# Optimization experiments

Hardware: AMD Instinct MI355X
Metric: run time of the kernel (lower is better)

## Reference

```python
import jax, jax.numpy as jnp
import numpy as np

EPS = 1e-5

def conv1d(x, w, b, stride, pad):
    # x: [N, Cin, L], w: [Cout, Cin, K]
    out = jax.lax.conv_general_dilated(x, w, (stride,), [(pad, pad)], dimension_numbers=('NCH', 'OIH', 'NCH'))
    return out + b[None, :, None]

def bn_eval(x, g, b):
    # BatchNorm1d in eval mode with running_mean=0, running_var=1
    return x * (g / jnp.sqrt(1.0 + EPS))[None, :, None] + b[None, :, None]

def maxpool3(x):
    return jax.lax.reduce_window(x, -jnp.inf, jax.lax.max, (1, 1, 3), (1, 1, 3), 'VALID')

def layer_norm(x, g, b):
    m = x.mean(-1, keepdims=True)
    v = ((x - m) ** 2).mean(-1, keepdims=True)
    return (x - m) / jnp.sqrt(v + EPS) * g + b

def lstm_dir(x, w_ih, w_hh, b_ih, b_hh, reverse):
    # x: [B, S, I]; torch gate order i, f, g, o
    B = x.shape[0]; H = w_hh.shape[1]
    xs = jnp.einsum('bsi,gi->bsg', x, w_ih) + b_ih + b_hh
    if reverse:
        xs = xs[:, ::-1]
    def step(carry, xt):
        h, c = carry
        gates = xt + h @ w_hh.T
        i, f, g, o = jnp.split(gates, 4, axis=-1)
        c = jax.nn.sigmoid(f) * c + jax.nn.sigmoid(i) * jnp.tanh(g)
        h = jax.nn.sigmoid(o) * jnp.tanh(c)
        return (h, c), h
    init = (jnp.zeros((B, H), x.dtype), jnp.zeros((B, H), x.dtype))
    _, hs = jax.lax.scan(step, init, jnp.swapaxes(xs, 0, 1))
    hs = jnp.swapaxes(hs, 0, 1)
    return hs[:, ::-1] if reverse else hs

def setup_inputs() -> dict:
    key = jax.random.key(0)
    ks = iter(jax.random.split(key, 48))
    def rn(shape, s=0.05):
        return jax.random.normal(next(ks), shape, jnp.float32) * s
    B, S, C, T, F0, Hg, Hl, NC = 64, 20, 8, 3000, 64, 128, 256, 5
    return dict(
        x=jax.random.normal(next(ks), (B, S, C, T), jnp.float32),
        edge_index=jax.random.randint(next(ks), (2, 56), 0, C, jnp.int32),
        conv1_w=rn((16, 1, 7)), conv1_b=jnp.zeros(16), bn1_g=jnp.ones(16), bn1_b=jnp.zeros(16),
        conv2_w=rn((32, 16, 5)), conv2_b=jnp.zeros(32), bn2_g=jnp.ones(32), bn2_b=jnp.zeros(32),
        conv3_w=rn((F0, 32, 3)), conv3_b=jnp.zeros(F0), bn3_g=jnp.ones(F0), bn3_b=jnp.zeros(F0),
        gcn0_w=rn((Hg, F0)), gcn0_b=jnp.zeros(Hg),
        gcn1_w=rn((Hg, Hg)), gcn1_b=jnp.zeros(Hg),
        gnn_ln_g=jnp.ones(Hg), gnn_ln_b=jnp.zeros(Hg),
        w_ih_l0=rn((4 * Hl, Hg)), w_hh_l0=rn((4 * Hl, Hl)), b_ih_l0=jnp.zeros(4 * Hl), b_hh_l0=jnp.zeros(4 * Hl),
        w_ih_l0r=rn((4 * Hl, Hg)), w_hh_l0r=rn((4 * Hl, Hl)), b_ih_l0r=jnp.zeros(4 * Hl), b_hh_l0r=jnp.zeros(4 * Hl),
        w_ih_l1=rn((4 * Hl, 2 * Hl)), w_hh_l1=rn((4 * Hl, Hl)), b_ih_l1=jnp.zeros(4 * Hl), b_hh_l1=jnp.zeros(4 * Hl),
        w_ih_l1r=rn((4 * Hl, 2 * Hl)), w_hh_l1r=rn((4 * Hl, Hl)), b_ih_l1r=jnp.zeros(4 * Hl), b_hh_l1r=jnp.zeros(4 * Hl),
        lstm_ln_g=jnp.ones(2 * Hl), lstm_ln_b=jnp.zeros(2 * Hl),
        cls_w=rn((NC, 2 * Hl)), cls_b=jnp.zeros(NC),
    )

def reference(x, edge_index, conv1_w, conv1_b, bn1_g, bn1_b, conv2_w, conv2_b, bn2_g, bn2_b, conv3_w, conv3_b, bn3_g, bn3_b, gcn0_w, gcn0_b, gcn1_w, gcn1_b, gnn_ln_g, gnn_ln_b, w_ih_l0, w_hh_l0, b_ih_l0, b_hh_l0, w_ih_l0r, w_hh_l0r, b_ih_l0r, b_hh_l0r, w_ih_l1, w_hh_l1, b_ih_l1, b_hh_l1, w_ih_l1r, w_hh_l1r, b_ih_l1r, b_hh_l1r, lstm_ln_g, lstm_ln_b, cls_w, cls_b):
    B, S, C, T = x.shape
    # batched per-channel CNN over all B*S epochs at once (original: python double loop)
    h = x.reshape(B * S * C, 1, T)
    h = maxpool3(jax.nn.relu(bn_eval(conv1d(h, conv1_w, conv1_b, 2, 3), bn1_g, bn1_b)))
    h = maxpool3(jax.nn.relu(bn_eval(conv1d(h, conv2_w, conv2_b, 2, 2), bn2_g, bn2_b)))
    h = jax.nn.relu(bn_eval(conv1d(h, conv3_w, conv3_b, 1, 1), bn3_g, bn3_b))
    feats = h.mean(-1).reshape(B * S, C, -1)  # AdaptiveAvgPool1d(1) -> [BS, C, 64]
    # GCNConv normalized adjacency: D^-1/2 (A + I) D^-1/2, graph is tiny (C nodes) so dense is exact and efficient
    src, dst = edge_index[0], edge_index[1]
    A = jnp.zeros((C, C), x.dtype).at[dst, src].add(1.0) + jnp.eye(C, dtype=x.dtype)
    dinv = 1.0 / jnp.sqrt(A.sum(1))
    An = A * dinv[:, None] * dinv[None, :]
    g1 = jax.nn.relu(jnp.einsum('ij,bjf->bif', An, feats @ gcn0_w.T) + gcn0_b)  # dropout off (eval)
    g2 = jnp.einsum('ij,bjf->bif', An, g1 @ gcn1_w.T) + gcn1_b
    g2 = layer_norm(g2, gnn_ln_g, gnn_ln_b)
    emb = g2.mean(1).reshape(B, S, -1)  # mean over nodes -> [B, S, 128]
    l0 = jnp.concatenate([lstm_dir(emb, w_ih_l0, w_hh_l0, b_ih_l0, b_hh_l0, False),
                          lstm_dir(emb, w_ih_l0r, w_hh_l0r, b_ih_l0r, b_hh_l0r, True)], -1)
    l1 = jnp.concatenate([lstm_dir(l0, w_ih_l1, w_hh_l1, b_ih_l1, b_hh_l1, False),
                          lstm_dir(l0, w_ih_l1r, w_hh_l1r, b_ih_l1r, b_hh_l1r, True)], -1)
    out = layer_norm(l1, lstm_ln_g, lstm_ln_b)
    return out @ cls_w.T + cls_b  # [B, S, 5]
```

## Files before the change

kernel.cpp:

```cpp
#include <hip/hip_runtime.h>
#include <hip/hip_bf16.h>

#define DEVI __device__ __forceinline__

typedef _Float16 h2f16 __attribute__((ext_vector_type(2)));
typedef _Float16 f16x4 __attribute__((ext_vector_type(4)));
typedef _Float16 f16x8 __attribute__((ext_vector_type(8)));
typedef float    f32x4 __attribute__((ext_vector_type(4)));
union U4H { uint4 u; h2f16 h[4]; };
union F8  { f16x8 v8; f16x4 v4[2]; };

DEVI float sigf(float x){ return 1.f/(1.f + __expf(-x)); }
DEVI float tanh_f(float x){
  float ax = fabsf(x);
  float e = __expf(-2.f*ax);
  float t = (1.f - e)/(1.f + e);
  return copysignf(t, x);
}
DEVI h2f16 hmax2(h2f16 a, h2f16 b){
  h2f16 r; r[0] = a[0] > b[0] ? a[0] : b[0]; r[1] = a[1] > b[1] ? a[1] : b[1]; return r;
}

__global__ __launch_bounds__(256) void k_prep(
  const int* __restrict__ ei, float* __restrict__ An,
  const float* __restrict__ w2, const float* __restrict__ w3,
  const float* __restrict__ bg2, const float* __restrict__ bg3,
  _Float16* __restrict__ bw2f, _Float16* __restrict__ bw3f,
  const float* __restrict__ a0, const float* __restrict__ a1,
  const float* __restrict__ a2, const float* __restrict__ a3,
  const float* __restrict__ a4, const float* __restrict__ a5,
  _Float16* __restrict__ o0, _Float16* __restrict__ o1,
  _Float16* __restrict__ o2, _Float16* __restrict__ o3,
  _Float16* __restrict__ o4, _Float16* __restrict__ o5,
  const float* __restrict__ whh0, const float* __restrict__ whh0r,
  const float* __restrict__ whh1, const float* __restrict__ whh1r,
  h2f16* __restrict__ wt0f, h2f16* __restrict__ wt0r,
  h2f16* __restrict__ wt1f, h2f16* __restrict__ wt1r)
{
  const int bid = blockIdx.x, tid = threadIdx.x;
  if (bid == 0){
    __shared__ float A[64];
    __shared__ float dinv[8];
    if (tid<64) A[tid] = ((tid>>3)==(tid&7)) ? 1.f : 0.f;
    __syncthreads();
    if (tid==0){
      for (int e=0;e<56;e++){ int s=ei[e], d=ei[56+e]; A[d*8+s] += 1.f; }
    }
    __syncthreads();
    if (tid<8){ float s=0.f; for (int j=0;j<8;j++) s+=A[tid*8+j]; dinv[tid]=rsqrtf(s); }
    __syncthreads();
    if (tid<64) An[tid] = A[tid]*dinv[tid>>3]*dinv[tid&7];
    return;
  }
  if (bid <= 24){
    const int i = (bid-1)*256 + tid;
    const float rs = rsqrtf(1.f+1e-5f);
    if (i < 3072){
      const int j = i&7, m = (i>>3)&15, g = (i>>7)&3, nt = (i>>9)&1, s = i>>10;
      const int kk = 32*s + 8*g + j;
      const int k = kk >> 4, ic = kk & 15, oc = nt*16 + m;
      bw2f[i] = (_Float16)((k < 5 ? w2[oc*80 + ic*5 + k] : 0.f) * (bg2[oc]*rs));
    }
    if (i < 6144){
      const int j = i&7, m = (i>>3)&15, g = (i>>7)&3, wv = (i>>9)&3, s = i>>11;
      const int kk = 32*s + 8*g + j;
      const int k = kk >> 5, ic = kk & 31, oc = wv*16 + m;
      bw3f[i] = (_Float16)(w3[oc*96 + ic*3 + k] * (bg3[oc]*rs));
    }
    return;
  }
  if (bid <= 5240){
    const int i = (bid-25)*256 + tid;
    if      (i <  131072) o0[i] = (_Float16)a0[i];
    else if (i <  262144) o1[i-131072] = (_Float16)a1[i-131072];
    else if (i <  786432) o2[i-262144] = (_Float16)a2[i-262144];
    else if (i < 1310720) o3[i-786432] = (_Float16)a3[i-786432];
    else if (i < 1318912) o4[i-1310720] = (_Float16)a4[i-1310720];
    else if (i < 1335296) o5[i-1318912] = (_Float16)a5[i-1318912];
    return;
  }
  {
    const int idx = (bid-5241)*256 + tid;
    const int which = idx >> 17, i = idx & 131071;
    const int g = i & 1023, jp = i >> 10;
    const float* in = (which==0) ? whh0 : (which==1) ? whh0r : (which==2) ? whh1 : whh1r;
    h2f16* outp    = (which==0) ? wt0f : (which==1) ? wt0r  : (which==2) ? wt1f : wt1r;
    h2f16 p;
    p[0] = (_Float16)in[g*256 + 2*jp];
    p[1] = (_Float16)in[g*256 + 2*jp + 1];
    outp[(long)jp*1024 + g] = p;
  }
}

__global__ __launch_bounds__(512,8) void k_conv(
    const float* __restrict__ x,
    const float* __restrict__ w1g, const float* __restrict__ c1b,
    const float* __restrict__ bg1, const float* __restrict__ bb1,
    const _Float16* __restrict__ bw2f,
    const float* __restrict__ c2b, const float* __restrict__ bg2, const float* __restrict__ bb2,
    const _Float16* __restrict__ bw3f,
    const float* __restrict__ c3b, const float* __restrict__ bg3, const float* __restrict__ bb3,
    _Float16* __restrict__ feats)
{
  __shared__ __align__(16) unsigned char smb[38592];
  __shared__ h2f16 w1p[16][4];
  __shared__ float kb1o[16], kb2o[32], kb3o[64];
  __shared__ float redc[8][16];
  h2f16* sxh = reinterpret_cast<h2f16*>(smb + 20160);
  const int tid = threadIdx.x;
  const long sig = blockIdx.x;
  const float* xg = x + sig*3000;

  {
    const float4* xg4 = reinterpret_cast<const float4*>(xg);
    for (int i=tid; i<750; i+=512){
      float4 v = xg4[i];
      h2f16 p0; p0[0]=(_Float16)v.x; p0[1]=(_Float16)v.y;
      h2f16 p1; p1[0]=(_Float16)v.z; p1[1]=(_Float16)v.w;
      sxh[2*i+2] = p0; sxh[2*i+3] = p1;
    }
    if (tid<3){
      h2f16 z; z[0]=(_Float16)0.f; z[1]=(_Float16)0.f;
      sxh[tid<2 ? tid : 1502] = z;
    }
    if (tid<32){
      const int rr = tid>>3, cp = tid&7;
      const int row = (rr<2) ? rr : (500+rr);
      h2f16 z; z[0]=(_Float16)0.f; z[1]=(_Float16)0.f;
      *reinterpret_cast<h2f16*>(smb + row*40 + 4*cp) = z;
    }
    const float rs = rsqrtf(1.f+1e-5f);
    if (tid<64){
      const int c = tid>>2, j = tid&3;
      const float s = bg1[c]*rs;
      h2f16 p;
      if (j==0){ p[0]=(_Float16)0.f; p[1]=(_Float16)(w1g[c*7+0]*s); }
      else     { p[0]=(_Float16)(w1g[c*7+2*j-1]*s); p[1]=(_Float16)(w1g[c*7+2*j]*s); }
      w1p[c][j] = p;
    }
    if (tid<16) kb1o[tid] = c1b[tid]*(bg1[tid]*rs) + bb1[tid];
    if (tid<32) kb2o[tid] = c2b[tid]*(bg2[tid]*rs) + bb2[tid];
    if (tid<64) kb3o[tid] = c3b[tid]*(bg3[tid]*rs) + bb3[tid];
  }
  __syncthreads();

  {
    const int cp = tid & 7;
    h2f16 wpa[4], wpb[4];
    #pragma unroll
    for (int j=0;j<4;j++){ wpa[j] = w1p[2*cp][j]; wpb[j] = w1p[2*cp+1][j]; }
    const float oa = kb1o[2*cp], ob = kb1o[2*cp+1];
    for (int u = tid>>3; u<500; u+=64){
      h2f16 xq[6];
      #pragma unroll
      for (int r=0;r<6;r++) xq[r] = sxh[3*u + r];
      float a0=0.f,a1=0.f,a2=0.f,b0=0.f,b1=0.f,b2=0.f;
      #pragma unroll
      for (int j=0;j<4;j++){
        a0 = __builtin_amdgcn_fdot2(xq[j],   wpa[j], a0, false);
        a1 = __builtin_amdgcn_fdot2(xq[j+1], wpa[j], a1, false);
        a2 = __builtin_amdgcn_fdot2(xq[j+2], wpa[j], a2, false);
        b0 = __builtin_amdgcn_fdot2(xq[j],   wpb[j], b0, false);
        b1 = __builtin_amdgcn_fdot2(xq[j+1], wpb[j], b1, false);
        b2 = __builtin_amdgcn_fdot2(xq[j+2], wpb[j], b2, false);
      }
      const float ya = fmaxf(fmaxf(fmaxf(a0,a1),a2) + oa, 0.f);
      const float yb = fmaxf(fmaxf(fmaxf(b0,b1),b2) + ob, 0.f);
      h2f16 p; p[0]=(_Float16)ya; p[1]=(_Float16)yb;
      *reinterpret_cast<h2f16*>(smb + (u+2)*40 + 4*cp) = p;
    }
  }
  __syncthreads();

  const int wv = tid >> 6, lane = tid & 63;
  const int m = lane & 15, g = lane >> 4;

  {
    const int nt = wv & 1;
    f16x8 bf[3];
    #pragma unroll
    for (int s=0;s<3;s++)
      bf[s] = *reinterpret_cast<const f16x8*>(&bw2f[(((s*2+nt)*4+g)*16+m)*8]);
    const int oc = nt*16 + m;
    const float of = kb2o[oc];
    #pragma unroll
    for (int i=0;i<4;i++){
      const int mt = (wv>>1) + 4*i;
      const int trow = mt*16 + m;
      f32x4 acc = {0.f,0.f,0.f,0.f};
      #pragma unroll
      for (int s=0;s<3;s++){
        const int kk = 32*s + 8*g;
        const int k = kk >> 4;
        const int ab = 80*trow + 40*k + 16*(g&1);
        F8 a;
        a.v4[0] = *reinterpret_cast<const f16x4*>(smb + ab);
        a.v4[1] = *reinterpret_cast<const f16x4*>(smb + ab + 8);
        acc = __builtin_amdgcn_mfma_f32_16x16x32_f16(a.v8, bf[s], acc, 0,0,0);
      }
      #pragma unroll
      for (int r=0;r<4;r++){
        const int t = mt*16 + 4*g + r;
        const float z = fmaxf(acc[r] + of, 0.f);
        *reinterpret_cast<_Float16*>(smb + 20160 + t*72 + 2*oc) = (_Float16)z;
      }
    }
  }
  __syncthreads();

  {
    if (tid < 240){
      const int rr = tid >> 4, cc = tid & 15;
      const int row = (rr == 0) ? 0 : (83 + rr);
      h2f16 z; z[0]=(_Float16)0.f; z[1]=(_Float16)0.f;
      *reinterpret_cast<h2f16*>(smb + row*80 + 4*cc) = z;
    }
    for (int i=tid; i<1328; i+=512){
      const int u = i >> 4, cc = i & 15;
      h2f16 a = *reinterpret_cast<const h2f16*>(smb + 20160 + (3*u)*72 + 4*cc);
      h2f16 b = *reinterpret_cast<const h2f16*>(smb + 20160 + (3*u+1)*72 + 4*cc);
      h2f16 c = *reinterpret_cast<const h2f16*>(smb + 20160 + (3*u+2)*72 + 4*cc);
      *reinterpret_cast<h2f16*>(smb + (u+1)*80 + 4*cc) = hmax2(hmax2(a,b), c);
    }
  }
  __syncthreads();

  {
    const int nt = wv & 3;
    f16x8 bf[3];
    #pragma unroll
    for (int s=0;s<3;s++)
      bf[s] = *reinterpret_cast<const f16x8*>(&bw3f[(((s*4+nt)*4+g)*16+m)*8]);
    const int oc = nt*16 + m;
    const float of = kb3o[oc];
    float macc = 0.f;
    #pragma unroll
    for (int q=0;q<3;q++){
      const int mt = (wv>>2) + 2*q;
      const int trow = mt*16 + m;
      f32x4 acc = {0.f,0.f,0.f,0.f};
      #pragma unroll
      for (int s=0;s<3;s++){
        f16x8 af = *reinterpret_cast<const f16x8*>(smb + (trow + s)*80 + 16*g);
        acc = __builtin_amdgcn_mfma_f32_16x16x32_f16(af, bf[s], acc, 0,0,0);
      }
      #pragma unroll
      for (int r=0;r<4;r++){
        const int t = mt*16 + 4*g + r;
        if (t < 83) macc += fmaxf(acc[r] + of, 0.f);
      }
    }
    macc += __shfl_xor(macc, 16);
    macc += __shfl_xor(macc, 32);
    if (lane < 16) redc[wv][m] = macc;
  }
  __syncthreads();
  if (tid < 64)
    feats[sig*64 + tid] = (_Float16)((redc[tid>>4][tid&15] + redc[(tid>>4)+4][tid&15]) * (1.f/83.f));
}

__global__ __launch_bounds__(256) void k_gcn1(
  const _Float16* __restrict__ X, const _Float16* __restrict__ W,
  const float* __restrict__ An, const float* __restrict__ b0,
  _Float16* __restrict__ g1, int K)
{
  __shared__ __align__(16) unsigned char lds[17408];
  __shared__ float ans[64];
  unsigned char* Xs = lds;
  unsigned char* Ws = lds + 4608;
  float* Cs = reinterpret_cast<float*>(lds);
  const int tid = threadIdx.x;
  const int m0 = blockIdx.y*64, n0 = blockIdx.x*64;
  const int wv = tid>>6, lane = tid&63, m = lane&15, g = lane>>4;
  const int sr = tid>>2, sq = tid&3;
  if (tid<64) ans[tid] = An[tid];
  f32x4 acc[4] = {{0.f,0.f,0.f,0.f},{0.f,0.f,0.f,0.f},{0.f,0.f,0.f,0.f},{0.f,0.f,0.f,0.f}};
  for (int k0=0; k0<K; k0+=32){
    uint4 xa = *reinterpret_cast<const uint4*>(X + (long)(m0+sr)*K + k0 + sq*8);
    uint4 wa = *reinterpret_cast<const uint4*>(W + (long)(n0+sr)*K + k0 + sq*8);
    __syncthreads();
    *reinterpret_cast<uint4*>(Xs + sr*72 + sq*16) = xa;
    *reinterpret_cast<uint4*>(Ws + sr*72 + sq*16) = wa;
    __syncthreads();
    f16x8 af = *reinterpret_cast<const f16x8*>(Xs + (wv*16+m)*72 + g*16);
    #pragma unroll
    for (int nt=0;nt<4;nt++){
      f16x8 bf = *reinterpret_cast<const f16x8*>(Ws + (nt*16+m)*72 + g*16);
      acc[nt] = __builtin_amdgcn_mfma_f32_16x16x32_f16(af, bf, acc[nt], 0,0,0);
    }
  }
  __syncthreads();
  #pragma unroll
  for (int nt=0;nt<4;nt++)
    #pragma unroll
    for (int r=0;r<4;r++)
      Cs[(wv*16 + g*4 + r)*68 + nt*16 + m] = acc[nt][r];
  __syncthreads();
  for (int idx=tid; idx<512; idx+=256){
    const int gg = idx>>6, j = idx&63;
    float t[8];
    #pragma unroll
    for (int c=0;c<8;c++) t[c] = Cs[(gg*8+c)*68 + j];
    const float bj = b0[n0+j];
    #pragma unroll
    for (int i=0;i<8;i++){
      float s = bj;
      #pragma unroll
      for (int c=0;c<8;c++) s += ans[i*8+c]*t[c];
      g1[(long)(m0 + gg*8 + i)*128 + n0 + j] = (_Float16)fmaxf(s, 0.f);
    }
  }
}

__global__ __launch_bounds__(256) void k_gcn2(
  const _Float16* __restrict__ X, const _Float16* __restrict__ W,
  const float* __restrict__ An, const float* __restrict__ b1,
  const float* __restrict__ lng, const float* __restrict__ lnb,
  _Float16* __restrict__ emb)
{
  __shared__ __align__(16) unsigned char lds[33792];
  __shared__ float ans[64];
  unsigned char* Xs = lds;
  unsigned char* Ws = lds + 4608;
  float* Cs = reinterpret_cast<float*>(lds);
  const int tid = threadIdx.x;
  const int m0 = blockIdx.x*64;
  const int wv = tid>>6, lane = tid&63, m = lane&15, g = lane>>4;
  const int sr = tid>>2, sq = tid&3;
  if (tid<64) ans[tid] = An[tid];
  f32x4 acc[8] = {};
  for (int k0=0; k0<128; k0+=32){
    uint4 xa = *reinterpret_cast<const uint4*>(X + (long)(m0+sr)*128 + k0 + sq*8);
    uint4 wa0 = *reinterpret_cast<const uint4*>(W + (long)(tid>>1)*128 + k0 + (tid&1)*16);
    uint4 wa1 = *reinterpret_cast<const uint4*>(W + (long)(tid>>1)*128 + k0 + (tid&1)*16 + 8);
    __syncthreads();
    *reinterpret_cast<uint4*>(Xs + sr*72 + sq*16) = xa;
    *reinterpret_cast<uint4*>(Ws + (tid>>1)*72 + (tid&1)*32) = wa0;
    *reinterpret_cast<uint4*>(Ws + (tid>>1)*72 + (tid&1)*32 + 16) = wa1;
    __syncthreads();
    f16x8 af = *reinterpret_cast<const f16x8*>(Xs + (wv*16+m)*72 + g*16);
    #pragma unroll
    for (int nt=0;nt<8;nt++){
      f16x8 bf = *reinterpret_cast<const f16x8*>(Ws + (nt*16+m)*72 + g*16);
      acc[nt] = __builtin_amdgcn_mfma_f32_16x16x32_f16(af, bf, acc[nt], 0,0,0);
    }
  }
  __syncthreads();
  #pragma unroll
  for (int nt=0;nt<8;nt++)
    #pragma unroll
    for (int r=0;r<4;r++)
      Cs[(wv*16 + g*4 + r)*132 + nt*16 + m] = acc[nt][r];
  __syncthreads();
  {
    const int s = tid>>5, l = tid&31;
    float g2v[8][4];
    #pragma unroll
    for (int jj=0;jj<4;jj++){
      const int j = l + jj*32;
      float t[8];
      #pragma unroll
      for (int c=0;c<8;c++) t[c] = Cs[(s*8+c)*132 + j];
      const float bj = b1[j];
      #pragma unroll
      for (int i=0;i<8;i++){
        float v = bj;
        #pragma unroll
        for (int c=0;c<8;c++) v += ans[i*8+c]*t[c];
        g2v[i][jj] = v;
      }
    }
    float mi[8], ri[8];
    #pragma unroll
    for (int i=0;i<8;i++){
      float sm=0.f, sq2=0.f;
      #pragma unroll
      for (int jj=0;jj<4;jj++){ sm += g2v[i][jj]; sq2 += g2v[i][jj]*g2v[i][jj]; }
      #pragma unroll
      for (int off=16; off>=1; off>>=1){ sm += __shfl_xor(sm, off); sq2 += __shfl_xor(sq2, off); }
      const float mu = sm*(1.f/128.f);
      mi[i] = mu;
      ri[i] = rsqrtf(sq2*(1.f/128.f) - mu*mu + 1e-5f);
    }
    #pragma unroll
    for (int jj=0;jj<4;jj++){
      const int j = l + jj*32;
      float a = 0.f;
      #pragma unroll
      for (int i=0;i<8;i++) a += (g2v[i][jj]-mi[i])*ri[i];
      emb[(long)(blockIdx.x*8 + s)*128 + j] = (_Float16)(lng[j]*a*0.125f + lnb[j]);
    }
  }
}

__global__ __launch_bounds__(256) void k_gemm_mf2(
  const _Float16* __restrict__ X,
  const _Float16* __restrict__ Wa, const _Float16* __restrict__ Wb,
  const float* __restrict__ b1a, const float* __restrict__ b2a,
  const float* __restrict__ b1b, const float* __restrict__ b2b,
  float* __restrict__ C, int co, int M, int N, int K, int ldc)
{
  __shared__ __align__(16) unsigned char lds[128*72];
  unsigned char* Xs = lds;
  unsigned char* Ws = lds + 64*72;
  const int z = blockIdx.z;
  const _Float16* W = z ? Wb : Wa;
  const float* b1 = z ? b1b : b1a;
  const float* b2 = z ? b2b : b2a;
  float* Cz = C + (z ? co : 0);
  const int tid = threadIdx.x;
  const int m0 = blockIdx.y*64, n0 = blockIdx.x*64;
  const int wv = tid>>6, lane = tid&63, m = lane&15, g = lane>>4;
  const int sr = tid>>2, sq = tid&3;
  f32x4 acc[4] = {{0.f,0.f,0.f,0.f},{0.f,0.f,0.f,0.f},{0.f,0.f,0.f,0.f},{0.f,0.f,0.f,0.f}};
  for (int k0=0; k0<K; k0+=32){
    uint4 xa = *reinterpret_cast<const uint4*>(X + (long)(m0+sr)*K + k0 + sq*8);
    uint4 wa = *reinterpret_cast<const uint4*>(W + (long)(n0+sr)*K + k0 + sq*8);
    __syncthreads();
    *reinterpret_cast<uint4*>(Xs + sr*72 + sq*16) = xa;
    *reinterpret_cast<uint4*>(Ws + sr*72 + sq*16) = wa;
    __syncthreads();
    f16x8 af = *reinterpret_cast<const f16x8*>(Xs + (wv*16+m)*72 + g*16);
    #pragma unroll
    for (int nt=0;nt<4;nt++){
      f16x8 bf = *reinterpret_cast<const f16x8*>(Ws + (nt*16+m)*72 + g*16);
      acc[nt] = __builtin_amdgcn_mfma_f32_16x16x32_f16(af, bf, acc[nt], 0,0,0);
    }
  }
  #pragma unroll
  for (int nt=0;nt<4;nt++){
    const int col = n0 + nt*16 + m;
    float bias = b1[col] + b2[col];
    #pragma unroll
    for (int r=0;r<4;r++)
      Cz[(long)(m0 + wv*16 + g*4 + r)*ldc + col] = acc[nt][r] + bias;
  }
}

__global__ __launch_bounds__(1024) void k_lstm(
    const float* __restrict__ xs,
    const h2f16* __restrict__ wtf,
    const h2f16* __restrict__ wtr,
    float* __restrict__ outf,
    _Float16* __restrict__ outh)
{
  const int S = 20;
  const int b = blockIdx.x >> 1, dir = blockIdx.x & 1;
  const h2f16* wt = dir ? wtr : wtf;
  __shared__ float part[4][1024];
  __shared__ _Float16 hsh[256];
  __shared__ __align__(16) unsigned char wlds[131072];
  const int tid = threadIdx.x;
  const int jg = tid >> 8, r = tid & 255, grow = r*4;
  uint4 wreg[16];
  #pragma unroll
  for (int jp=0;jp<16;jp++)
    wreg[jp] = *reinterpret_cast<const uint4*>(
        reinterpret_cast<const unsigned int*>(wt + (long)(jg*32+jp)*1024 + grow));
  {
    const uint4* wsrc = reinterpret_cast<const uint4*>(wt);
    uint4* wdst = reinterpret_cast<uint4*>(wlds);
    for (int i=tid; i<8192; i+=1024){
      const int src = (i < 4096) ? (4096 + i) : (12288 + (i - 4096));
      wdst[i] = wsrc[src];
    }
  }
  if (tid < 256) hsh[tid] = (_Float16)0.f;
  float cc = 0.f;
  __syncthreads();
  const h2f16* hp2 = reinterpret_cast<const h2f16*>(hsh);
  for (int st=0; st<S; ++st){
    const int t = dir ? (S-1-st) : st;
    float a0=0.f,a1=0.f,a2=0.f,a3=0.f;
    #pragma unroll
    for (int jp=0; jp<16; ++jp){
      const h2f16 hv = hp2[jg*32 + jp];
      U4H w; w.u = wreg[jp];
      a0 = __builtin_amdgcn_fdot2(hv, w.h[0], a0, false);
      a1 = __builtin_amdgcn_fdot2(hv, w.h[1], a1, false);
      a2 = __builtin_amdgcn_fdot2(hv, w.h[2], a2, false);
      a3 = __builtin_amdgcn_fdot2(hv, w.h[3], a3, false);
    }
    if (jg < 2){
      #pragma unroll 8
      for (int jp=16; jp<32; ++jp){
        const h2f16 hv = hp2[jg*32 + jp];
        U4H w; w.u = *reinterpret_cast<const uint4*>(
            wlds + (long)(jg*16 + (jp-16))*4096 + grow*4);
        a0 = __builtin_amdgcn_fdot2(hv, w.h[0], a0, false);
        a1 = __builtin_amdgcn_fdot2(hv, w.h[1], a1, false);
        a2 = __builtin_amdgcn_fdot2(hv, w.h[2], a2, false);
        a3 = __builtin_amdgcn_fdot2(hv, w.h[3], a3, false);
      }
    } else {
      #pragma unroll 8
      for (int jp=16; jp<32; ++jp){
        const h2f16 hv = hp2[jg*32 + jp];
        U4H w; w.u = *reinterpret_cast<const uint4*>(
            reinterpret_cast<const unsigned int*>(wt + (long)(jg*32+jp)*1024 + grow));
        a0 = __builtin_amdgcn_fdot2(hv, w.h[0], a0, false);
        a1 = __builtin_amdgcn_fdot2(hv, w.h[1], a1, false);
        a2 = __builtin_amdgcn_fdot2(hv, w.h[2], a2, false);
        a3 = __builtin_amdgcn_fdot2(hv, w.h[3], a3, false);
      }
    }
    *reinterpret_cast<float4*>(&part[jg][grow]) = make_float4(a0,a1,a2,a3);
    __syncthreads();
    if (tid < 256){
      const float* xrow = xs + ((long)b*S + t)*2048 + dir*1024;
      float g0 = xrow[tid]
               + (part[0][tid]      + part[1][tid])      + (part[2][tid]      + part[3][tid]);
      float g1 = xrow[256+tid]
               + (part[0][256+tid]  + part[1][256+tid])  + (part[2][256+tid]  + part[3][256+tid]);
      float g2 = xrow[512+tid]
               + (part[0][512+tid]  + part[1][512+tid])  + (part[2][512+tid]  + part[3][512+tid]);
      float g3 = xrow[768+tid]
               + (part[0][768+tid]  + part[1][768+tid])  + (part[2][768+tid]  + part[3][768+tid]);
      cc = sigf(g1)*cc + sigf(g0)*tanh_f(g2);
      const float h = sigf(g3)*tanh_f(cc);
      hsh[tid] = (_Float16)h;
      const long o = ((long)b*S + t)*512 + dir*256 + tid;
      if (outf) outf[o] = h;
      if (outh) outh[o] = (_Float16)h;
    }
    __syncthreads();
  }
}

__global__ __launch_bounds__(128) void k_lncls(
  const float* __restrict__ in, const float* __restrict__ g,
  const float* __restrict__ b, const float* __restrict__ cw,
  const float* __restrict__ cb, float* __restrict__ out)
{
  const int row = blockIdx.x, tid = threadIdx.x;
  __shared__ float sred[4];
  __shared__ float cred[2][5];
  float4 v = *reinterpret_cast<const float4*>(in + (long)row*512 + tid*4);
  float s  = v.x+v.y+v.z+v.w;
  float sq = v.x*v.x+v.y*v.y+v.z*v.z+v.w*v.w;
  #pragma unroll
  for (int off=32; off>=1; off>>=1){ s += __shfl_xor(s, off); sq += __shfl_xor(sq, off); }
  const int wv = tid>>6;
  if ((tid&63)==0){ sred[wv*2]=s; sred[wv*2+1]=sq; }
  __syncthreads();
  const float S = sred[0]+sred[2], SQ = sred[1]+sred[3];
  const float m = S*(1.f/512.f);
  const float rstd = rsqrtf(SQ*(1.f/512.f) - m*m + 1e-5f);
  float4 gg = *reinterpret_cast<const float4*>(g + tid*4);
  float4 bb = *reinterpret_cast<const float4*>(b + tid*4);
  const float n0 = (v.x-m)*rstd*gg.x + bb.x;
  const float n1 = (v.y-m)*rstd*gg.y + bb.y;
  const float n2 = (v.z-m)*rstd*gg.z + bb.z;
  const float n3 = (v.w-m)*rstd*gg.w + bb.w;
  #pragma unroll
  for (int nc=0; nc<5; ++nc){
    float4 w = *reinterpret_cast<const float4*>(cw + nc*512 + tid*4);
    float p = n0*w.x + n1*w.y + n2*w.z + n3*w.w;
    #pragma unroll
    for (int off=32; off>=1; off>>=1) p += __shfl_xor(p, off);
    if ((tid&63)==0) cred[wv][nc] = p;
  }
  __syncthreads();
  if (tid < 5) out[(long)row*5 + tid] = cred[0][tid] + cred[1][tid] + cb[tid];
}

extern "C" void kernel_launch(void* const* d_in, const int* in_sizes, int n_in,
                              void* d_out, int out_size, void* d_ws, size_t ws_size,
                              hipStream_t stream)
{
  const float* x     = (const float*)d_in[0];
  const int*   ei    = (const int*)d_in[1];
  const float* w1    = (const float*)d_in[2];
  const float* c1b   = (const float*)d_in[3];
  const float* bg1   = (const float*)d_in[4];
  const float* bb1   = (const float*)d_in[5];
  const float* w2    = (const float*)d_in[6];
  const float* c2b   = (const float*)d_in[7];
  const float* bg2   = (const float*)d_in[8];
  const float* bb2   = (const float*)d_in[9];
  const float* w3    = (const float*)d_in[10];
  const float* c3b   = (const float*)d_in[11];
  const float* bg3   = (const float*)d_in[12];
  const float* bb3   = (const float*)d_in[13];
  const float* gcn0w = (const float*)d_in[14];
  const float* gcn0b = (const float*)d_in[15];
  const float* gcn1w = (const float*)d_in[16];
  const float* gcn1b = (const float*)d_in[17];
  const float* lng   = (const float*)d_in[18];
  const float* lnb   = (const float*)d_in[19];
  const float* wih0  = (const float*)d_in[20];
  const float* whh0  = (const float*)d_in[21];
  const float* bih0  = (const float*)d_in[22];
  const float* bhh0  = (const float*)d_in[23];
  const float* wih0r = (const float*)d_in[24];
  const float* whh0r = (const float*)d_in[25];
  const float* bih0r = (const float*)d_in[26];
  const float* bhh0r = (const float*)d_in[27];
  const float* wih1  = (const float*)d_in[28];
  const float* whh1  = (const float*)d_in[29];
  const float* bih1  = (const float*)d_in[30];
  const float* bhh1  = (const float*)d_in[31];
  const float* wih1r = (const float*)d_in[32];
  const float* whh1r = (const float*)d_in[33];
  const float* bih1r = (const float*)d_in[34];
  const float* bhh1r = (const float*)d_in[35];
  const float* lstmg = (const float*)d_in[36];
  const float* lstmb = (const float*)d_in[37];
  const float* clsw  = (const float*)d_in[38];
  const float* clsb  = (const float*)d_in[39];
  float* ws  = (float*)d_ws;
  float* out = (float*)d_out;

  float*    An      = ws + 0;
  _Float16* bw2f    = (_Float16*)(ws + 64);
  _Float16* bw3f    = (_Float16*)(ws + 1600);
  _Float16* feats16 = (_Float16*)(ws + 4672);
  _Float16* g1b16   = (_Float16*)(ws + 332352);
  _Float16* emb16   = (_Float16*)(ws + 987712);
  _Float16* l0h     = (_Float16*)(ws + 1069632);
  _Float16* w0f     = (_Float16*)(ws + 1397312);
  _Float16* w0rf    = (_Float16*)(ws + 1462848);
  _Float16* w1f     = (_Float16*)(ws + 1528384);
  _Float16* w1rf    = (_Float16*)(ws + 1790528);
  _Float16* gw0f    = (_Float16*)(ws + 2052672);
  _Float16* gw1f    = (_Float16*)(ws + 2056768);
  h2f16*    wt0f    = (h2f16*)(ws + 2064960);
  h2f16*    wt0r    = (h2f16*)(ws + 2196032);
  h2f16*    wt1f    = (h2f16*)(ws + 2327104);
  h2f16*    wt1r    = (h2f16*)(ws + 2458176);
  float*    l1f     = ws + 2589248;
  float*    xs      = ws + 3244608;

  k_prep<<<7289, 256, 0, stream>>>(ei, An, w2, w3, bg2, bg3, bw2f, bw3f,
                                   wih0, wih0r, wih1, wih1r, gcn0w, gcn1w,
                                   w0f, w0rf, w1f, w1rf, gw0f, gw1f,
                                   whh0, whh0r, whh1, whh1r,
                                   wt0f, wt0r, wt1f, wt1r);
  k_conv<<<10240, 512, 0, stream>>>(x, w1,c1b,bg1,bb1, bw2f,c2b,bg2,bb2,
                                    bw3f,c3b,bg3,bb3, feats16);

  k_gcn1<<<dim3(2, 160), 256, 0, stream>>>(feats16, gw0f, An, gcn0b, g1b16, 64);
  k_gcn2<<<160, 256, 0, stream>>>(g1b16, gw1f, An, gcn1b, lng, lnb, emb16);

  k_gemm_mf2<<<dim3(16, 20, 2), 256, 0, stream>>>(emb16, w0f, w0rf,
      bih0, bhh0, bih0r, bhh0r, xs, 1024, 1280, 1024, 128, 2048);
  k_lstm<<<128, 1024, 0, stream>>>(xs, wt0f, wt0r, nullptr, l0h);

  k_gemm_mf2<<<dim3(16, 20, 2), 256, 0, stream>>>(l0h, w1f, w1rf,
      bih1, bhh1, bih1r, bhh1r, xs, 1024, 1280, 1024, 512, 2048);
  k_lstm<<<128, 1024, 0, stream>>>(xs, wt1f, wt1r, l1f, nullptr);

  k_lncls<<<1280, 128, 0, stream>>>(l1f, lstmg, lstmb, clsw, clsb, out);
}
```

Before: 293.1 us.

## Fuse GCN layers, store LSTM gate inputs in fp16, tile weight transpose

The two GCN kernels become one, which keeps the intermediate layer in LDS instead of writing it to global memory. The input-projection GEMM now uses 128-row tiles with 512 threads and writes fp16 gate pre-activations, and the LSTM kernels read them as fp16. This halves that traffic but reduces precision. The recurrent-weight transpose in the prep kernel now goes through an LDS tile so global reads are coalesced, and the launch uses fewer blocks.

```diff
diff --git a/kernel.cpp b/kernel.cpp
--- a/kernel.cpp
+++ b/kernel.cpp
@@ -80,15 +80,28 @@
     return;
   }
   {
-    const int idx = (bid-5241)*256 + tid;
-    const int which = idx >> 17, i = idx & 131071;
-    const int g = i & 1023, jp = i >> 10;
+    __shared__ float tl[64][65];
+    const int t = bid - 5241;
+    const int which = t >> 6, tile = t & 63;
+    const int tg = tile >> 2, tc = tile & 3;
     const float* in = (which==0) ? whh0 : (which==1) ? whh0r : (which==2) ? whh1 : whh1r;
     h2f16* outp    = (which==0) ? wt0f : (which==1) ? wt0r  : (which==2) ? wt1f : wt1r;
-    h2f16 p;
-    p[0] = (_Float16)in[g*256 + 2*jp];
-    p[1] = (_Float16)in[g*256 + 2*jp + 1];
-    outp[(long)jp*1024 + g] = p;
+    #pragma unroll
+    for (int p=0;p<16;p++){
+      const int lin = p*256 + tid;
+      const int r = lin >> 6, cc = lin & 63;
+      tl[r][cc] = in[(tg*64 + r)*256 + tc*64 + cc];
+    }
+    __syncthreads();
+    #pragma unroll
+    for (int p=0;p<8;p++){
+      const int lin = p*256 + tid;
+      const int gl = lin & 63, jph = lin >> 6;
+      h2f16 v;
+      v[0] = (_Float16)tl[gl][2*jph];
+      v[1] = (_Float16)tl[gl][2*jph+1];
+      outp[(long)(tc*32 + jph)*1024 + tg*64 + gl] = v;
+    }
   }
 }
 
@@ -259,98 +272,90 @@
     feats[sig*64 + tid] = (_Float16)((redc[tid>>4][tid&15] + redc[(tid>>4)+4][tid&15]) * (1.f/83.f));
 }
 
-__global__ __launch_bounds__(256) void k_gcn1(
-  const _Float16* __restrict__ X, const _Float16* __restrict__ W,
+__global__ __launch_bounds__(256) void k_gcn(
+  const _Float16* __restrict__ feats, const _Float16* __restrict__ W0,
+  const _Float16* __restrict__ W1,
   const float* __restrict__ An, const float* __restrict__ b0,
-  _Float16* __restrict__ g1, int K)
+  const float* __restrict__ b1, const float* __restrict__ lng,
+  const float* __restrict__ lnb, _Float16* __restrict__ emb)
 {
-  __shared__ __align__(16) unsigned char lds[17408];
+  __shared__ __align__(16) unsigned char lds[66304];
   __shared__ float ans[64];
-  unsigned char* Xs = lds;
-  unsigned char* Ws = lds + 4608;
-  float* Cs = reinterpret_cast<float*>(lds);
-  const int tid = threadIdx.x;
-  const int m0 = blockIdx.y*64, n0 = blockIdx.x*64;
-  const int wv = tid>>6, lane = tid&63, m = lane&15, g = lane>>4;
-  const int sr = tid>>2, sq = tid&3;
-  if (tid<64) ans[tid] = An[tid];
-  f32x4 acc[4] = {{0.f,0.f,0.f,0.f},{0.f,0.f,0.f,0.f},{0.f,0.f,0.f,0.f},{0.f,0.f,0.f,0.f}};
-  for (int k0=0; k0<K; k0+=32){
-    uint4 xa = *reinterpret_cast<const uint4*>(X + (long)(m0+sr)*K + k0 + sq*8);
-    uint4 wa = *reinterpret_cast<const uint4*>(W + (long)(n0+sr)*K + k0 + sq*8);
-    __syncthreads();
-    *reinterpret_cast<uint4*>(Xs + sr*72 + sq*16) = xa;
-    *reinterpret_cast<uint4*>(Ws + sr*72 + sq*16) = wa;
-    __syncthreads();
-    f16x8 af = *reinterpret_cast<const f16x8*>(Xs + (wv*16+m)*72 + g*16);
-    #pragma unroll
-    for (int nt=0;nt<4;nt++){
-      f16x8 bf = *reinterpret_cast<const f16x8*>(Ws + (nt*16+m)*72 + g*16);
-      acc[nt] = __builtin_amdgcn_mfma_f32_16x16x32_f16(af, bf, acc[nt], 0,0,0);
-    }
-  }
-  __syncthreads();
-  #pragma unroll
-  for (int nt=0;nt<4;nt++)
-    #pragma unroll
-    for (int r=0;r<4;r++)
-      Cs[(wv*16 + g*4 + r)*68 + nt*16 + m] = acc[nt][r];
-  __syncthreads();
-  for (int idx=tid; idx<512; idx+=256){
-    const int gg = idx>>6, j = idx&63;
-    float t[8];
-    #pragma unroll
-    for (int c=0;c<8;c++) t[c] = Cs[(gg*8+c)*68 + j];
-    const float bj = b0[n0+j];
-    #pragma unroll
-    for (int i=0;i<8;i++){
-      float s = bj;
-      #pragma unroll
-      for (int c=0;c<8;c++) s += ans[i*8+c]*t[c];
-      g1[(long)(m0 + gg*8 + i)*128 + n0 + j] = (_Float16)fmaxf(s, 0.f);
-    }
-  }
-}
-
-__global__ __launch_bounds__(256) void k_gcn2(
-  const _Float16* __restrict__ X, const _Float16* __restrict__ W,
-  const float* __restrict__ An, const float* __restrict__ b1,
-  const float* __restrict__ lng, const float* __restrict__ lnb,
-  _Float16* __restrict__ emb)
-{
-  __shared__ __align__(16) unsigned char lds[33792];
-  __shared__ float ans[64];
-  unsigned char* Xs = lds;
-  unsigned char* Ws = lds + 4608;
-  float* Cs = reinterpret_cast<float*>(lds);
+  unsigned char* Xs  = lds;
+  unsigned char* Ws0 = lds + 4608;
+  float*         Cs  = reinterpret_cast<float*>(lds + 13824);
+  unsigned char* W1s = lds + 13824;
+  unsigned char* g1h = lds + 48896;
   const int tid = threadIdx.x;
   const int m0 = blockIdx.x*64;
   const int wv = tid>>6, lane = tid&63, m = lane&15, g = lane>>4;
   const int sr = tid>>2, sq = tid&3;
   if (tid<64) ans[tid] = An[tid];
-  f32x4 acc[8] = {};
-  for (int k0=0; k0<128; k0+=32){
-    uint4 xa = *reinterpret_cast<const uint4*>(X + (long)(m0+sr)*128 + k0 + sq*8);
-    uint4 wa0 = *reinterpret_cast<const uint4*>(W + (long)(tid>>1)*128 + k0 + (tid&1)*16);
-    uint4 wa1 = *reinterpret_cast<const uint4*>(W + (long)(tid>>1)*128 + k0 + (tid&1)*16 + 8);
-    __syncthreads();
-    *reinterpret_cast<uint4*>(Xs + sr*72 + sq*16) = xa;
-    *reinterpret_cast<uint4*>(Ws + (tid>>1)*72 + (tid&1)*32) = wa0;
-    *reinterpret_cast<uint4*>(Ws + (tid>>1)*72 + (tid&1)*32 + 16) = wa1;
-    __syncthreads();
-    f16x8 af = *reinterpret_cast<const f16x8*>(Xs + (wv*16+m)*72 + g*16);
-    #pragma unroll
-    for (int nt=0;nt<8;nt++){
-      f16x8 bf = *reinterpret_cast<const f16x8*>(Ws + (nt*16+m)*72 + g*16);
-      acc[nt] = __builtin_amdgcn_mfma_f32_16x16x32_f16(af, bf, acc[nt], 0,0,0);
-    }
-  }
-  __syncthreads();
-  #pragma unroll
-  for (int nt=0;nt<8;nt++)
-    #pragma unroll
-    for (int r=0;r<4;r++)
-      Cs[(wv*16 + g*4 + r)*132 + nt*16 + m] = acc[nt][r];
+  {
+    f32x4 acc[8] = {};
+    for (int k0=0; k0<64; k0+=32){
+      uint4 xa  = *reinterpret_cast<const uint4*>(feats + (long)(m0+sr)*64 + k0 + sq*8);
+      uint4 wa0 = *reinterpret_cast<const uint4*>(W0 + (long)sr*64 + k0 + sq*8);
+      uint4 wa1 = *reinterpret_cast<const uint4*>(W0 + (long)(sr+64)*64 + k0 + sq*8);
+      __syncthreads();
+      *reinterpret_cast<uint4*>(Xs + sr*72 + sq*16) = xa;
+      *reinterpret_cast<uint4*>(Ws0 + sr*72 + sq*16) = wa0;
+      *reinterpret_cast<uint4*>(Ws0 + (sr+64)*72 + sq*16) = wa1;
+      __syncthreads();
+      f16x8 af = *reinterpret_cast<const f16x8*>(Xs + (wv*16+m)*72 + g*16);
+      #pragma unroll
+      for (int nt=0;nt<8;nt++){
+        f16x8 bf = *reinterpret_cast<const f16x8*>(Ws0 + (nt*16+m)*72 + g*16);
+        acc[nt] = __builtin_amdgcn_mfma_f32_16x16x32_f16(af, bf, acc[nt], 0,0,0);
+      }
+    }
+    __syncthreads();
+    #pragma unroll
+    for (int nt=0;nt<8;nt++)
+      #pragma unroll
+      for (int r=0;r<4;r++)
+        Cs[(wv*16 + g*4 + r)*132 + nt*16 + m] = acc[nt][r];
+  }
+  __syncthreads();
+  for (int idx=tid; idx<1024; idx+=256){
+    const int gg = idx>>7, j = idx&127;
+    float t[8];
+    #pragma unroll
+    for (int c=0;c<8;c++) t[c] = Cs[(gg*8+c)*132 + j];
+    const float bj = b0[j];
+    #pragma unroll
+    for (int i=0;i<8;i++){
+      float s = bj;
+      #pragma unroll
+      for (int c=0;c<8;c++) s += ans[i*8+c]*t[c];
+      *reinterpret_cast<_Float16*>(g1h + (gg*8+i)*272 + j*2) = (_Float16)fmaxf(s, 0.f);
+    }
+  }
+  __syncthreads();
+  for (int i2=tid; i2<2048; i2+=256){
+    const int row = i2>>4, q = i2&15;
+    *reinterpret_cast<uint4*>(W1s + row*272 + q*16) =
+        *reinterpret_cast<const uint4*>(W1 + (long)row*128 + q*8);
+  }
+  __syncthreads();
+  {
+    f32x4 acc2[8] = {};
+    #pragma unroll
+    for (int kc=0;kc<4;kc++){
+      f16x8 af = *reinterpret_cast<const f16x8*>(g1h + (wv*16+m)*272 + kc*64 + g*16);
+      #pragma unroll
+      for (int nt=0;nt<8;nt++){
+        f16x8 bf = *reinterpret_cast<const f16x8*>(W1s + (nt*16+m)*272 + kc*64 + g*16);
+        acc2[nt] = __builtin_amdgcn_mfma_f32_16x16x32_f16(af, bf, acc2[nt], 0,0,0);
+      }
+    }
+    __syncthreads();
+    #pragma unroll
+    for (int nt=0;nt<8;nt++)
+      #pragma unroll
+      for (int r=0;r<4;r++)
+        Cs[(wv*16 + g*4 + r)*132 + nt*16 + m] = acc2[nt][r];
+  }
   __syncthreads();
   {
     const int s = tid>>5, l = tid&31;
@@ -393,32 +398,34 @@
   }
 }
 
-__global__ __launch_bounds__(256) void k_gemm_mf2(
+__global__ __launch_bounds__(512) void k_gemm_mf2(
   const _Float16* __restrict__ X,
   const _Float16* __restrict__ Wa, const _Float16* __restrict__ Wb,
   const float* __restrict__ b1a, const float* __restrict__ b2a,
   const float* __restrict__ b1b, const float* __restrict__ b2b,
-  float* __restrict__ C, int co, int M, int N, int K, int ldc)
+  _Float16* __restrict__ C, int K)
 {
-  __shared__ __align__(16) unsigned char lds[128*72];
+  __shared__ __align__(16) unsigned char lds[13824];
   unsigned char* Xs = lds;
-  unsigned char* Ws = lds + 64*72;
+  unsigned char* Ws = lds + 9216;
   const int z = blockIdx.z;
   const _Float16* W = z ? Wb : Wa;
   const float* b1 = z ? b1b : b1a;
   const float* b2 = z ? b2b : b2a;
-  float* Cz = C + (z ? co : 0);
+  _Float16* Cz = C + (z ? 1024 : 0);
   const int tid = threadIdx.x;
-  const int m0 = blockIdx.y*64, n0 = blockIdx.x*64;
+  const int m0 = blockIdx.y*128, n0 = blockIdx.x*64;
   const int wv = tid>>6, lane = tid&63, m = lane&15, g = lane>>4;
   const int sr = tid>>2, sq = tid&3;
   f32x4 acc[4] = {{0.f,0.f,0.f,0.f},{0.f,0.f,0.f,0.f},{0.f,0.f,0.f,0.f},{0.f,0.f,0.f,0.f}};
   for (int k0=0; k0<K; k0+=32){
     uint4 xa = *reinterpret_cast<const uint4*>(X + (long)(m0+sr)*K + k0 + sq*8);
-    uint4 wa = *reinterpret_cast<const uint4*>(W + (long)(n0+sr)*K + k0 + sq*8);
+    uint4 wa = make_uint4(0,0,0,0);
+    if (tid < 256)
+      wa = *reinterpret_cast<const uint4*>(W + (long)(n0+sr)*K + k0 + sq*8);
     __syncthreads();
     *reinterpret_cast<uint4*>(Xs + sr*72 + sq*16) = xa;
-    *reinterpret_cast<uint4*>(Ws + sr*72 + sq*16) = wa;
+    if (tid < 256) *reinterpret_cast<uint4*>(Ws + sr*72 + sq*16) = wa;
     __syncthreads();
     f16x8 af = *reinterpret_cast<const f16x8*>(Xs + (wv*16+m)*72 + g*16);
     #pragma unroll
@@ -433,12 +440,12 @@
     float bias = b1[col] + b2[col];
     #pragma unroll
     for (int r=0;r<4;r++)
-      Cz[(long)(m0 + wv*16 + g*4 + r)*ldc + col] = acc[nt][r] + bias;
+      Cz[(long)(m0 + wv*16 + g*4 + r)*2048 + col] = (_Float16)(acc[nt][r] + bias);
   }
 }
 
 __global__ __launch_bounds__(1024) void k_lstm(
-    const float* __restrict__ xs,
+    const _Float16* __restrict__ xs,
     const h2f16* __restrict__ wtf,
     const h2f16* __restrict__ wtr,
     float* __restrict__ outf,
@@ -507,14 +514,14 @@
     *reinterpret_cast<float4*>(&part[jg][grow]) = make_float4(a0,a1,a2,a3);
     __syncthreads();
     if (tid < 256){
-      const float* xrow = xs + ((long)b*S + t)*2048 + dir*1024;
-      float g0 = xrow[tid]
+      const _Float16* xrow = xs + ((long)b*S + t)*2048 + dir*1024;
+      float g0 = (float)xrow[tid]
                + (part[0][tid]      + part[1][tid])      + (part[2][tid]      + part[3][tid]);
-      float g1 = xrow[256+tid]
+      float g1 = (float)xrow[256+tid]
                + (part[0][256+tid]  + part[1][256+tid])  + (part[2][256+tid]  + part[3][256+tid]);
-      float g2 = xrow[512+tid]
+      float g2 = (float)xrow[512+tid]
                + (part[0][512+tid]  + part[1][512+tid])  + (part[2][512+tid]  + part[3][512+tid]);
-      float g3 = xrow[768+tid]
+      float g3 = (float)xrow[768+tid]
                + (part[0][768+tid]  + part[1][768+tid])  + (part[2][768+tid]  + part[3][768+tid]);
       cc = sigf(g1)*cc + sigf(g0)*tanh_f(g2);
       const float h = sigf(g3)*tanh_f(cc);
@@ -629,9 +636,9 @@
   h2f16*    wt1f    = (h2f16*)(ws + 2327104);
   h2f16*    wt1r    = (h2f16*)(ws + 2458176);
   float*    l1f     = ws + 2589248;
-  float*    xs      = ws + 3244608;
-
-  k_prep<<<7289, 256, 0, stream>>>(ei, An, w2, w3, bg2, bg3, bw2f, bw3f,
+  _Float16* xsh     = (_Float16*)(ws + 3244608);
+
+  k_prep<<<5497, 256, 0, stream>>>(ei, An, w2, w3, bg2, bg3, bw2f, bw3f,
                                    wih0, wih0r, wih1, wih1r, gcn0w, gcn1w,
                                    w0f, w0rf, w1f, w1rf, gw0f, gw1f,
                                    whh0, whh0r, whh1, whh1r,
@@ -639,16 +646,16 @@
   k_conv<<<10240, 512, 0, stream>>>(x, w1,c1b,bg1,bb1, bw2f,c2b,bg2,bb2,
                                     bw3f,c3b,bg3,bb3, feats16);
 
-  k_gcn1<<<dim3(2, 160), 256, 0, stream>>>(feats16, gw0f, An, gcn0b, g1b16, 64);
-  k_gcn2<<<160, 256, 0, stream>>>(g1b16, gw1f, An, gcn1b, lng, lnb, emb16);
-
-  k_gemm_mf2<<<dim3(16, 20, 2), 256, 0, stream>>>(emb16, w0f, w0rf,
-      bih0, bhh0, bih0r, bhh0r, xs, 1024, 1280, 1024, 128, 2048);
-  k_lstm<<<128, 1024, 0, stream>>>(xs, wt0f, wt0r, nullptr, l0h);
-
-  k_gemm_mf2<<<dim3(16, 20, 2), 256, 0, stream>>>(l0h, w1f, w1rf,
-      bih1, bhh1, bih1r, bhh1r, xs, 1024, 1280, 1024, 512, 2048);
-  k_lstm<<<128, 1024, 0, stream>>>(xs, wt1f, wt1r, l1f, nullptr);
+  k_gcn<<<160, 256, 0, stream>>>(feats16, gw0f, gw1f, An, gcn0b, gcn1b,
+                                 lng, lnb, emb16);
+
+  k_gemm_mf2<<<dim3(16, 10, 2), 512, 0, stream>>>(emb16, w0f, w0rf,
+      bih0, bhh0, bih0r, bhh0r, xsh, 128);
+  k_lstm<<<128, 1024, 0, stream>>>(xsh, wt0f, wt0r, nullptr, l0h);
+
+  k_gemm_mf2<<<dim3(16, 10, 2), 512, 0, stream>>>(l0h, w1f, w1rf,
+      bih1, bhh1, bih1r, bhh1r, xsh, 512);
+  k_lstm<<<128, 1024, 0, stream>>>(xsh, wt1f, wt1r, l1f, nullptr);
 
   k_lncls<<<1280, 128, 0, stream>>>(l1f, lstmg, lstmb, clsw, clsb, out);
 }
```

Result: no change. 296.5 us (+1.2%).
